# Kernel optimization log

Hardware: AMD Instinct MI355X
Metric: run time of the kernel (lower is better)

## Reference

```python
import jax, jax.numpy as jnp
import numpy as np


def derived_adjustedmean(activation_in, carry_in):
    # avnn.derives.derived_adjustedmean: per-sample scalar derived from the
    # activator and carry channels. Assumed: average of the two channel means.
    return 0.5 * (jnp.mean(activation_in, axis=-1) + jnp.mean(carry_in, axis=-1))


def setup_inputs() -> dict:
    key = jax.random.key(0)
    k1, k2, k3 = jax.random.split(key, 3)
    B, D_IN, D_OUT = 2048, 4096, 4096
    x = jax.random.normal(k1, (B, D_IN, 2), dtype=jnp.float32)
    # nn.Linear default init scale ~ 1/sqrt(fan_in)
    scale = 1.0 / np.sqrt(D_IN)
    W = jax.random.uniform(k2, (D_OUT, D_IN), dtype=jnp.float32, minval=-scale, maxval=scale)
    b = jax.random.uniform(k3, (D_OUT,), dtype=jnp.float32, minval=-scale, maxval=scale)
    return {"x": x, "W": W, "b": b}


def reference(x, W, b):
    # x: [B, D_in, 2] -> channel 0 = activator, channel 1 = carry
    activation_in = x[..., 0]           # [B, D_in]
    carry_in = x[..., 1]                # [B, D_in]
    # Linear + ReLU on the activator channel
    activation_out = jax.nn.relu(jnp.einsum('bi,oi->bo', activation_in, W) + b)  # [B, D_out]
    # Vectorized replacement of the per-batch Python loop: per-row scalar derive,
    # broadcast-filled across the output features.
    val = derived_adjustedmean(activation_in, carry_in)            # [B]
    carry_out = jnp.broadcast_to(val[:, None], activation_out.shape)  # [B, D_out]
    return jnp.stack([activation_out, carry_out], axis=-1)         # [B, D_out, 2]
```

## Files before the change

### kernel.cpp

```cpp
#include <hip/hip_runtime.h>
#include <stdint.h>


typedef __bf16 bf16x8_t __attribute__((ext_vector_type(8)));
typedef float f32x4_t __attribute__((ext_vector_type(4)));
typedef __attribute__((address_space(1))) void gvoid_t;
typedef __attribute__((address_space(3))) void lvoid_t;

__device__ __forceinline__ uint32_t f32_to_bf16_rne(float f) {
    uint32_t u = __float_as_uint(f);
    return (u + 0x7fffu + ((u >> 16) & 1u)) >> 16;
}

__device__ __forceinline__ uint32_t swz(uint32_t b) {
    return b ^ (((b >> 7) & 7u) << 4);
}

__device__ __forceinline__ bf16x8_t ds_read128(uint32_t addr) {
    bf16x8_t d;
    asm volatile("ds_read_b128 %0, %1" : "=&v"(d) : "v"(addr));
    return d;
}

__global__ __launch_bounds__(256) void convert_x_frag(
    const float* __restrict__ src, uint4* __restrict__ dst,
    float* __restrict__ val, int K, int spb) {
    const int t = threadIdx.x;
    const int rbase = blockIdx.x * 16;
    const int r16 = t & 15, og = t >> 4;
    const int row = rbase + r16;
    const int ksn = K >> 5;
    const int strip = row >> 6, rfrag = (row >> 4) & 3;
    float s = 0.f;
    const int st0 = blockIdx.y * spb;
    for (int st = st0; st < st0 + spb; ++st) {
        const int o = og + st * 16;
        const int k = o * 8;
        uint32_t pk[4];
        const float4* p = (const float4*)(src + ((size_t)row * K + k) * 2);
#pragma unroll
        for (int i = 0; i < 4; ++i) {
            float4 v = p[i];
            s += (v.x + v.y) + (v.z + v.w);
            pk[i] = f32_to_bf16_rne(v.x) | (f32_to_bf16_rne(v.z) << 16);
        }
        const int ks = o >> 2;
        const int ln = r16 | ((o & 3) << 4);
        dst[((size_t)(strip * ksn + ks) * 4 + rfrag) * 64 + ln] =
            make_uint4(pk[0], pk[1], pk[2], pk[3]);
    }
    s += __shfl_xor(s, 16, 64);
    s += __shfl_xor(s, 32, 64);
    __shared__ float red[4][16];
    if ((t & 48) == 0) red[t >> 6][r16] = s;
    __syncthreads();
    if (t < 16) {
        float p = red[0][t] + red[1][t] + red[2][t] + red[3][t];
        atomicAdd(&val[rbase + t], p / (float)(2 * K));
    }
}

__global__ __launch_bounds__(256) void convert_w(
    const float4* __restrict__ w4, uint2* __restrict__ wbf, int n4) {
    const int i = blockIdx.x * 256 + threadIdx.x;
    if (i < n4) {
        float4 v = w4[i];
        uint2 p;
        p.x = f32_to_bf16_rne(v.x) | (f32_to_bf16_rne(v.y) << 16);
        p.y = f32_to_bf16_rne(v.z) | (f32_to_bf16_rne(v.w) << 16);
        wbf[i] = p;
    }
}

#define BKB 128
#define NSLAB 16384
#define LDS_BYTES (2 * NSLAB)

__global__ __launch_bounds__(256, 2) void gemm_hyb(
    const uint4* __restrict__ Af, const uint16_t* __restrict__ Wbf,
    const float* __restrict__ bias, const float* __restrict__ val,
    float* __restrict__ out, int M, int N, int K) {
    extern __shared__ char lds[];
    const uint32_t lds0 = (uint32_t)(uintptr_t)(lvoid_t*)lds;

    const int tid = threadIdx.x;
    const int wv = tid >> 6;
    const int lane = tid & 63;
    const int lrow = lane & 15, lkg = lane >> 4;
    const int nbx = N >> 7, nby = M >> 7;
    const int nwg = nbx * nby;

    int wg = blockIdx.x;
    if ((nwg & 7) == 0) {
        const int cpx = nwg >> 3;
        wg = (wg & 7) * cpx + (wg >> 3);
    }
    const int y = wg % nby, x = wg / nby;
    const int m0 = y * 128, n0 = x * 128;
    const int wr = wv >> 1, wc = wv & 1;

    uint32_t bsrc[4];
#pragma unroll
    for (int l = 0; l < 4; ++l) {
        uint32_t sb = swz((uint32_t)(l * 256 + tid) * 16u);
        bsrc[l] = (uint32_t)(n0 + (int)(sb >> 7)) * (uint32_t)(K * 2) + (sb & 127u);
    }
    uint32_t brd[4];
#pragma unroll
    for (int n = 0; n < 4; ++n)
        brd[n] = swz((uint32_t)(wc * 64 + n * 16 + lrow) * 128u + (uint32_t)(lkg * 16));

    const int ksn = K >> 5;
    const bf16x8_t* awp = (const bf16x8_t*)Af +
        ((size_t)((m0 >> 6) + wr) * ksn * 4) * 64 + lane;

    f32x4_t acc[4][4];
#pragma unroll
    for (int i = 0; i < 4; ++i)
#pragma unroll
        for (int j = 0; j < 4; ++j) acc[i][j] = (f32x4_t){0.f, 0.f, 0.f, 0.f};

    const int NT = K >> 6;
    bf16x8_t A0[8], A1[8];

#define LOADA(Ad, tt)                                                         \
    {                                                                         \
        const bf16x8_t* ap = awp + (size_t)(tt) * 512;                        \
        _Pragma("unroll") for (int q = 0; q < 8; ++q) Ad[q] = ap[q * 64];     \
    }
#define STAGE_B(tt)                                                           \
    {                                                                         \
        const int slot = (tt) & 1;                                            \
        _Pragma("unroll") for (int l = 0; l < 4; ++l) {                       \
            const char* src = (const char*)Wbf + bsrc[l] + (size_t)(tt) * BKB;\
            char* dst = lds + slot * NSLAB + l * 4096 + wv * 1024;            \
            __builtin_amdgcn_global_load_lds((gvoid_t*)src, (lvoid_t*)dst,    \
                                             16, 0, 0);                       \
        }                                                                     \
    }
#define TILE(tt, Ac, An)                                                      \
    {                                                                         \
        const uint32_t lb = lds0 + ((tt) & 1) * NSLAB;                        \
        if ((tt) + 1 < NT) { STAGE_B((tt) + 1); LOADA(An, (tt) + 1); }        \
        bf16x8_t b0[4], b1[4];                                                \
        _Pragma("unroll") for (int n = 0; n < 4; ++n)                         \
            b0[n] = ds_read128(lb + brd[n]);                                  \
        _Pragma("unroll") for (int n = 0; n < 4; ++n)                         \
            b1[n] = ds_read128(lb + (brd[n] ^ 64u));                          \
        asm volatile("s_waitcnt lgkmcnt(4)" ::: "memory");                    \
        __builtin_amdgcn_sched_barrier(0);                                    \
        __builtin_amdgcn_s_setprio(1);                                        \
        _Pragma("unroll") for (int m = 0; m < 4; ++m)                         \
            _Pragma("unroll") for (int n = 0; n < 4; ++n)                     \
                acc[m][n] = __builtin_amdgcn_mfma_f32_16x16x32_bf16(          \
                    Ac[m], b0[n], acc[m][n], 0, 0, 0);                        \
        __builtin_amdgcn_s_setprio(0);                                        \
        asm volatile("s_waitcnt lgkmcnt(0)" ::: "memory");                    \
        __builtin_amdgcn_sched_barrier(0);                                    \
        __builtin_amdgcn_s_setprio(1);                                        \
        _Pragma("unroll") for (int m = 0; m < 4; ++m)                         \
            _Pragma("unroll") for (int n = 0; n < 4; ++n)                     \
                acc[m][n] = __builtin_amdgcn_mfma_f32_16x16x32_bf16(          \
                    Ac[4 + m], b1[n], acc[m][n], 0, 0, 0);                    \
        __builtin_amdgcn_s_setprio(0);                                        \
        if ((tt) + 1 < NT) {                                                  \
            asm volatile("s_waitcnt vmcnt(0)" ::: "memory");                  \
            __builtin_amdgcn_sched_barrier(0);                                \
            __builtin_amdgcn_s_barrier();                                     \
        }                                                                     \
    }

    STAGE_B(0);
    LOADA(A0, 0);
    asm volatile("s_waitcnt vmcnt(0)" ::: "memory");
    __builtin_amdgcn_sched_barrier(0);
    __builtin_amdgcn_s_barrier();

    for (int t = 0; t < NT; t += 2) {
        TILE(t, A0, A1);
        if (t + 1 < NT) TILE(t + 1, A1, A0);
    }
#undef LOADA
#undef STAGE_B
#undef TILE

    const int gmb = m0 + wr * 64;
    const int gnb = n0 + wc * 64;
    float bcol[4];
#pragma unroll
    for (int n = 0; n < 4; ++n) bcol[n] = bias[gnb + n * 16 + lrow];
#pragma unroll
    for (int m = 0; m < 4; ++m) {
#pragma unroll
        for (int r = 0; r < 4; ++r) {
            const int row = gmb + m * 16 + lkg * 4 + r;
            const float vr = val[row];
            float2* orow = (float2*)(out + (size_t)row * N * 2);
#pragma unroll
            for (int n = 0; n < 4; ++n) {
                const int col = gnb + n * 16 + lrow;
                float a = fmaxf(acc[m][n][r] + bcol[n], 0.f);
                orow[col] = make_float2(a, vr);
            }
        }
    }
}

__global__ __launch_bounds__(256) void convert_x_stats(
    const float4* __restrict__ x4, uint32_t* __restrict__ abf,
    float* __restrict__ val, int din) {
    const int row = blockIdx.x;
    const int t = threadIdx.x;
    const int f4pr = din >> 1;
    const float4* xr = x4 + (size_t)row * f4pr;
    float s = 0.f;
    for (int i = t; i < f4pr; i += 256) {
        float4 v = xr[i];
        s += (v.x + v.y) + (v.z + v.w);
    }
#pragma unroll
    for (int off = 32; off; off >>= 1) s += __shfl_down(s, off, 64);
    __shared__ float red[4];
    if ((t & 63) == 0) red[t >> 6] = s;
    __syncthreads();
    if (t == 0) val[row] = (red[0] + red[1] + red[2] + red[3]) / (float)(2 * din);
}

__global__ __launch_bounds__(256) void gemm_fallback(
    const float* __restrict__ xf, const float* __restrict__ Wf,
    const float* __restrict__ bias, const float* __restrict__ val,
    float* __restrict__ out, int M, int N, int K) {
    __shared__ uint16_t lA[128 * 32];
    __shared__ uint16_t lB[128 * 32];
    const int tid = threadIdx.x;
    const int wv = tid >> 6;
    const int lane = tid & 63;
    const int lrow = lane & 15;
    const int lkg = lane >> 4;
    const int m0 = blockIdx.y * 128;
    const int n0 = blockIdx.x * 128;
    const int wr = wv >> 1, wc = wv & 1;
    f32x4_t acc[4][4];
#pragma unroll
    for (int i = 0; i < 4; ++i)
#pragma unroll
        for (int j = 0; j < 4; ++j) acc[i][j] = (f32x4_t){0.f, 0.f, 0.f, 0.f};
    for (int k0 = 0; k0 < K; k0 += 32) {
        float4 va[8];
        float4 vb[4];
#pragma unroll
        for (int i = 0; i < 8; ++i) {
            const int p = i * 256 + tid;
            const int row = p >> 4, pc = p & 15;
            va[i] = *(const float4*)(xf + ((size_t)(m0 + row) * K + k0 + pc * 2) * 2);
        }
#pragma unroll
        for (int i = 0; i < 4; ++i) {
            const int q = i * 256 + tid;
            const int row = q >> 3, qc = q & 7;
            vb[i] = *(const float4*)(Wf + (size_t)(n0 + row) * K + k0 + qc * 4);
        }
        __syncthreads();
#pragma unroll
        for (int i = 0; i < 8; ++i) {
            const int p = i * 256 + tid;
            const int row = p >> 4, pc = p & 15;
            *(uint32_t*)&lA[row * 32 + pc * 2] =
                f32_to_bf16_rne(va[i].x) | (f32_to_bf16_rne(va[i].z) << 16);
        }
#pragma unroll
        for (int i = 0; i < 4; ++i) {
            const int q = i * 256 + tid;
            const int row = q >> 3, qc = q & 7;
            uint2 pk;
            pk.x = f32_to_bf16_rne(vb[i].x) | (f32_to_bf16_rne(vb[i].y) << 16);
            pk.y = f32_to_bf16_rne(vb[i].z) | (f32_to_bf16_rne(vb[i].w) << 16);
            *(uint2*)&lB[row * 32 + qc * 4] = pk;
        }
        __syncthreads();
        bf16x8_t af[4], bfr[4];
#pragma unroll
        for (int i = 0; i < 4; ++i)
            af[i] = *(const bf16x8_t*)&lA[(wr * 64 + i * 16 + lrow) * 32 + lkg * 8];
#pragma unroll
        for (int j = 0; j < 4; ++j)
            bfr[j] = *(const bf16x8_t*)&lB[(wc * 64 + j * 16 + lrow) * 32 + lkg * 8];
#pragma unroll
        for (int i = 0; i < 4; ++i)
#pragma unroll
            for (int j = 0; j < 4; ++j)
                acc[i][j] = __builtin_amdgcn_mfma_f32_16x16x32_bf16(af[i], bfr[j],
                                                                    acc[i][j], 0, 0, 0);
        __syncthreads();
    }
    const int gm = m0 + wr * 64;
    const int gn = n0 + wc * 64;
    float bcol[4];
#pragma unroll
    for (int j = 0; j < 4; ++j) bcol[j] = bias[gn + j * 16 + lrow];
#pragma unroll
    for (int i = 0; i < 4; ++i) {
#pragma unroll
        for (int r = 0; r < 4; ++r) {
            const int row = gm + i * 16 + lkg * 4 + r;
            const float vr = val[row];
            float2* orow = (float2*)(out + (size_t)row * N * 2);
#pragma unroll
            for (int j = 0; j < 4; ++j) {
                const int col = gn + j * 16 + lrow;
                float a = fmaxf(acc[i][j][r] + bcol[j], 0.f);
                orow[col] = make_float2(a, vr);
            }
        }
    }
}

extern "C" void kernel_launch(void* const* d_in, const int* in_sizes, int n_in,
                              void* d_out, int out_size, void* d_ws, size_t ws_size,
                              hipStream_t stream) {
    const float* x = (const float*)d_in[0];
    const float* W = (const float*)d_in[1];
    const float* b = (const float*)d_in[2];
    float* out = (float*)d_out;

    const int DOUT = in_sizes[2];
    const int DIN = in_sizes[1] / DOUT;
    const int B = in_sizes[0] / (2 * DIN);

    float* val = (float*)d_ws;
    const size_t aoff = 8192;
    const size_t abytes = (size_t)B * DIN * 2;
    const size_t wbytes = (size_t)DOUT * DIN * 2;
    const bool big = ws_size >= aoff + abytes + wbytes &&
                     (B % 128) == 0 && (DOUT % 128) == 0 && (DIN % 128) == 0;

    if (big) {
        uint4* abf = (uint4*)((char*)d_ws + aoff);
        uint32_t* wbf = (uint32_t*)((char*)d_ws + aoff + abytes);

        (void)hipMemsetAsync(val, 0, (size_t)B * sizeof(float), stream);

        const int osteps = DIN / 128;
        int split = 1;
        for (int c : {16, 8, 4, 2}) { if (osteps % c == 0) { split = c; break; } }
        const int spb = osteps / split;
        dim3 gx(B / 16, split);
        convert_x_frag<<<gx, 256, 0, stream>>>(x, abf, val, DIN, spb);

        const int n4 = DOUT * DIN / 4;
        convert_w<<<(n4 + 255) / 256, 256, 0, stream>>>((const float4*)W, (uint2*)wbf, n4);

        (void)hipFuncSetAttribute((const void*)gemm_hyb,
                                  hipFuncAttributeMaxDynamicSharedMemorySize, LDS_BYTES);
        const int nwg = (DOUT / 128) * (B / 128);
        gemm_hyb<<<nwg, 256, LDS_BYTES, stream>>>(abf, (const uint16_t*)wbf,
                                                  b, val, out, B, DOUT, DIN);
    } else {
        convert_x_stats<<<B, 256, 0, stream>>>((const float4*)x, nullptr, val, DIN);
        dim3 grid(DOUT / 128, B / 128);
        gemm_fallback<<<grid, 256, 0, stream>>>(x, W, b, val, out, B, DOUT, DIN);
    }
}
```

Baseline: 117.1 us.

## Triple-buffer W tiles in LDS and switch GEMM to plain 2D grid

The B-operand LDS staging goes from double to triple buffering, so W tiles are prefetched two iterations ahead. The wait before each barrier becomes a partial vmcnt that leaves the newest stage in flight. A loads now use inline-asm global_load_dwordx4 so their count is predictable for those vmcnt values. The XCD-aware workgroup remapping is dropped in favour of a plain 2D grid, which may hurt L2 locality, and the larger LDS footprint may limit occupancy.

Result: faster. 114.7 us (-2.1%).

```diff
diff --git a/kernel.cpp b/kernel.cpp
--- a/kernel.cpp
+++ b/kernel.cpp
@@ -19,6 +19,12 @@
 __device__ __forceinline__ bf16x8_t ds_read128(uint32_t addr) {
     bf16x8_t d;
     asm volatile("ds_read_b128 %0, %1" : "=&v"(d) : "v"(addr));
+    return d;
+}
+
+__device__ __forceinline__ bf16x8_t gload16(const void* p) {
+    bf16x8_t d;
+    asm volatile("global_load_dwordx4 %0, %1, off" : "=&v"(d) : "v"(p));
     return d;
 }
 
@@ -74,7 +80,7 @@
 
 #define BKB 128
 #define NSLAB 16384
-#define LDS_BYTES (2 * NSLAB)
+#define LDS_BYTES (3 * NSLAB)
 
 __global__ __launch_bounds__(256, 2) void gemm_hyb(
     const uint4* __restrict__ Af, const uint16_t* __restrict__ Wbf,
@@ -87,16 +93,8 @@
     const int wv = tid >> 6;
     const int lane = tid & 63;
     const int lrow = lane & 15, lkg = lane >> 4;
-    const int nbx = N >> 7, nby = M >> 7;
-    const int nwg = nbx * nby;
-
-    int wg = blockIdx.x;
-    if ((nwg & 7) == 0) {
-        const int cpx = nwg >> 3;
-        wg = (wg & 7) * cpx + (wg >> 3);
-    }
-    const int y = wg % nby, x = wg / nby;
-    const int m0 = y * 128, n0 = x * 128;
+    const int m0 = blockIdx.y * 128;
+    const int n0 = blockIdx.x * 128;
     const int wr = wv >> 1, wc = wv & 1;
 
     uint32_t bsrc[4];
@@ -111,8 +109,8 @@
         brd[n] = swz((uint32_t)(wc * 64 + n * 16 + lrow) * 128u + (uint32_t)(lkg * 16));
 
     const int ksn = K >> 5;
-    const bf16x8_t* awp = (const bf16x8_t*)Af +
-        ((size_t)((m0 >> 6) + wr) * ksn * 4) * 64 + lane;
+    const char* abase = (const char*)Af +
+        (((size_t)((m0 >> 6) + wr) * ksn * 4) * 64 + lane) * 16;
 
     f32x4_t acc[4][4];
 #pragma unroll
@@ -125,12 +123,13 @@
 
 #define LOADA(Ad, tt)                                                         \
     {                                                                         \
-        const bf16x8_t* ap = awp + (size_t)(tt) * 512;                        \
-        _Pragma("unroll") for (int q = 0; q < 8; ++q) Ad[q] = ap[q * 64];     \
+        const char* ap = abase + (size_t)(tt) * 8192;                         \
+        _Pragma("unroll") for (int q = 0; q < 8; ++q)                         \
+            Ad[q] = gload16(ap + q * 1024);                                   \
     }
 #define STAGE_B(tt)                                                           \
     {                                                                         \
-        const int slot = (tt) & 1;                                            \
+        const int slot = (tt) % 3;                                            \
         _Pragma("unroll") for (int l = 0; l < 4; ++l) {                       \
             const char* src = (const char*)Wbf + bsrc[l] + (size_t)(tt) * BKB;\
             char* dst = lds + slot * NSLAB + l * 4096 + wv * 1024;            \
@@ -140,8 +139,9 @@
     }
 #define TILE(tt, Ac, An)                                                      \
     {                                                                         \
-        const uint32_t lb = lds0 + ((tt) & 1) * NSLAB;                        \
-        if ((tt) + 1 < NT) { STAGE_B((tt) + 1); LOADA(An, (tt) + 1); }        \
+        if ((tt) + 1 < NT) LOADA(An, (tt) + 1);                               \
+        if ((tt) + 2 < NT) STAGE_B((tt) + 2);                                 \
+        const uint32_t lb = lds0 + ((tt) % 3) * NSLAB;                        \
         bf16x8_t b0[4], b1[4];                                                \
         _Pragma("unroll") for (int n = 0; n < 4; ++n)                         \
             b0[n] = ds_read128(lb + brd[n]);                                  \
@@ -164,7 +164,11 @@
                     Ac[4 + m], b1[n], acc[m][n], 0, 0, 0);                    \
         __builtin_amdgcn_s_setprio(0);                                        \
         if ((tt) + 1 < NT) {                                                  \
-            asm volatile("s_waitcnt vmcnt(0)" ::: "memory");                  \
+            if ((tt) + 2 < NT) {                                              \
+                asm volatile("s_waitcnt vmcnt(4)" ::: "memory");              \
+            } else {                                                          \
+                asm volatile("s_waitcnt vmcnt(0)" ::: "memory");              \
+            }                                                                 \
             __builtin_amdgcn_sched_barrier(0);                                \
             __builtin_amdgcn_s_barrier();                                     \
         }                                                                     \
@@ -172,7 +176,12 @@
 
     STAGE_B(0);
     LOADA(A0, 0);
-    asm volatile("s_waitcnt vmcnt(0)" ::: "memory");
+    if (NT > 1) {
+        STAGE_B(1);
+        asm volatile("s_waitcnt vmcnt(4)" ::: "memory");
+    } else {
+        asm volatile("s_waitcnt vmcnt(0)" ::: "memory");
+    }
     __builtin_amdgcn_sched_barrier(0);
     __builtin_amdgcn_s_barrier();
 
@@ -352,9 +361,9 @@
 
         (void)hipFuncSetAttribute((const void*)gemm_hyb,
                                   hipFuncAttributeMaxDynamicSharedMemorySize, LDS_BYTES);
-        const int nwg = (DOUT / 128) * (B / 128);
-        gemm_hyb<<<nwg, 256, LDS_BYTES, stream>>>(abf, (const uint16_t*)wbf,
-                                                  b, val, out, B, DOUT, DIN);
+        dim3 grid(DOUT / 128, B / 128);
+        gemm_hyb<<<grid, 256, LDS_BYTES, stream>>>(abf, (const uint16_t*)wbf,
+                                                   b, val, out, B, DOUT, DIN);
     } else {
         convert_x_stats<<<B, 256, 0, stream>>>((const float4*)x, nullptr, val, DIN);
         dim3 grid(DOUT / 128, B / 128);
```
